# Optimization experiments

Hardware: AMD Instinct MI355X
Metric: run time of the kernel (lower is better)

Reference implementation:

```python
import jax, jax.numpy as jnp
import numpy as np

B, IN, OUT = 8192, 1024, 1024


def setup_inputs() -> dict:
    key = jax.random.key(0)
    k1, k2 = jax.random.split(key)
    x = jax.random.normal(k1, (B, IN), dtype=jnp.float32)
    W_seed = jax.random.normal(k2, (IN, OUT), dtype=jnp.float32) / np.sqrt(IN).astype(np.float32)
    b_seed = jnp.zeros((OUT,), dtype=jnp.float32)
    W_sig = jnp.zeros((2,), dtype=jnp.float32)  # mixture logits over ['dense','Toeplitz']
    b_sig = jnp.zeros((2,), dtype=jnp.float32)  # mixture logits over ['dense','None']
    A_sig = jnp.zeros((2,), dtype=jnp.float32)  # mixture logits over ['linear','relu']
    return {"x": x, "W_seed": W_seed, "b_seed": b_seed,
            "W_sig": W_sig, "b_sig": b_sig, "A_sig": A_sig}


def _toeplitz_from_seed(W_seed):
    # seed_vec = [W_seed[0, out-1], ..., W_seed[0, 1], W_seed[0,0], ..., W_seed[in-1,0]]
    in_sz, out_sz = W_seed.shape
    seed_vec = jnp.concatenate([W_seed[0, -1:0:-1], W_seed[:, 0]])  # [out-1 + in]
    # W_toep[i, j] = seed_vec[i - j + out - 1]
    idx = jnp.arange(in_sz)[:, None] - jnp.arange(out_sz)[None, :] + (out_sz - 1)
    return seed_vec[idx]  # [in, out]


def reference(x, W_seed, b_seed, W_sig, b_sig, A_sig):
    W_toep = _toeplitz_from_seed(W_seed)
    w_s = jax.nn.softmax(W_sig)
    W_core = w_s[0] * W_seed + w_s[1] * W_toep          # softmax-weighted weight mixture
    b_s = jax.nn.softmax(b_sig)
    b_core = b_s[0] * b_seed                             # 'None' branch contributes zeros
    out = x @ W_core + b_core                            # [B, out]
    a_s = jax.nn.softmax(A_sig)
    return a_s[0] * out + a_s[1] * jax.nn.relu(out)      # activation mixture
```

## Files before the change

### kernel.cpp

```cpp
#include <hip/hip_runtime.h>

typedef unsigned short ushort_t;
typedef __bf16 bf16x8 __attribute__((ext_vector_type(8)));
typedef float f32x4 __attribute__((ext_vector_type(4)));

#define AS1 __attribute__((address_space(1)))
#define AS3 __attribute__((address_space(3)))

__device__ __forceinline__ ushort_t f2bf(float f) {
    unsigned u = __builtin_bit_cast(unsigned, f);
    u = (u + 0x7fffu + ((u >> 16) & 1u)) >> 16;
    return (ushort_t)u;
}

__device__ __forceinline__ void async16(void* lds, const void* g) {
    __builtin_amdgcn_global_load_lds((const AS1 unsigned int*)g,
                                     (AS3 unsigned int*)lds, 16, 0, 0);
}

__device__ __forceinline__ void softmax2(const float* __restrict__ sig, float& s0, float& s1) {
    float a = sig[0], b = sig[1];
    float m = fmaxf(a, b);
    float e0 = __expf(a - m), e1 = __expf(b - m);
    float inv = 1.0f / (e0 + e1);
    s0 = e0 * inv; s1 = e1 * inv;
}

__device__ __forceinline__ float toep_val(const float* __restrict__ Wseed, int k, int o) {
    return (k >= o) ? Wseed[(size_t)(k - o) << 10] : Wseed[o - k];
}

__global__ __launch_bounds__(256) void prep_kernel(const float* __restrict__ x,
                                                   const float* __restrict__ Wseed,
                                                   const float* __restrict__ Wsig,
                                                   ushort_t* __restrict__ xb,
                                                   ushort_t* __restrict__ Wt) {
    int b = blockIdx.x;
    if (b < 4096) {
        int i = b * 256 + threadIdx.x;
        const float4* xp = (const float4*)x + (size_t)i * 2;
        float4 a = xp[0], c = xp[1];
        uint4 r;
        r.x = (unsigned)f2bf(a.x) | ((unsigned)f2bf(a.y) << 16);
        r.y = (unsigned)f2bf(a.z) | ((unsigned)f2bf(a.w) << 16);
        r.z = (unsigned)f2bf(c.x) | ((unsigned)f2bf(c.y) << 16);
        r.w = (unsigned)f2bf(c.z) | ((unsigned)f2bf(c.w) << 16);
        ((uint4*)xb)[i] = r;
        return;
    }
    __shared__ float T[64][65];
    int bb = b - 4096;
    int k0 = (bb >> 4) * 64;
    int o0 = (bb & 15) * 64;
    int t = threadIdx.x;
    #pragma unroll
    for (int i = 0; i < 4; ++i) {
        int lin = t + i * 256;
        int kr = lin >> 4;
        int c4 = lin & 15;
        float4 v = *(const float4*)&Wseed[(size_t)(k0 + kr) * 1024 + o0 + c4 * 4];
        T[kr][c4 * 4 + 0] = v.x;
        T[kr][c4 * 4 + 1] = v.y;
        T[kr][c4 * 4 + 2] = v.z;
        T[kr][c4 * 4 + 3] = v.w;
    }
    __syncthreads();
    float s0, s1; softmax2(Wsig, s0, s1);
    #pragma unroll
    for (int i = 0; i < 2; ++i) {
        int lin = t + i * 256;
        int oo = lin >> 3;
        int kq = (lin & 7) * 8;
        unsigned r[4];
        #pragma unroll
        for (int q = 0; q < 4; ++q) {
            float v0 = s0 * T[kq + 2 * q + 0][oo] + s1 * toep_val(Wseed, k0 + kq + 2 * q + 0, o0 + oo);
            float v1 = s0 * T[kq + 2 * q + 1][oo] + s1 * toep_val(Wseed, k0 + kq + 2 * q + 1, o0 + oo);
            r[q] = (unsigned)f2bf(v0) | ((unsigned)f2bf(v1) << 16);
        }
        *(uint4*)&Wt[(size_t)(o0 + oo) * 1024 + k0 + kq] = make_uint4(r[0], r[1], r[2], r[3]);
    }
}

#define NKT 16

__global__ __launch_bounds__(512, 2) void gemm_kernel(const ushort_t* __restrict__ Xb,
                                                      const ushort_t* __restrict__ Wt,
                                                      const float* __restrict__ bseed,
                                                      const float* __restrict__ bsig,
                                                      const float* __restrict__ asig,
                                                      float* __restrict__ out) {
    __shared__ ushort_t lds[73728];
    ushort_t* p0 = lds;
    ushort_t* p1 = lds + 24576;
    ushort_t* p2 = lds + 49152;

    const int t = threadIdx.x;
    const int wv = t >> 6;
    const int lane = t & 63;

    const int orig = blockIdx.x;
    const int g = orig & 7;
    const int within = orig >> 3;
    const int rb = g * 4 + (within >> 3);
    const int cb = within & 7;
    const int brow = rb * 256;
    const int bcol = cb * 128;

    const int r0 = t >> 3;
    const int kcs = 8 * ((t & 7) ^ (r0 & 7));
    const ushort_t* gA = Xb + (size_t)(brow + r0) * 1024 + kcs;
    const ushort_t* gB = Wt + (size_t)(bcol + r0) * 1024 + kcs;

    const int wr = (wv >> 1) * 64;
    const int wcn = (wv & 1) * 64;
    const int fr = lane & 15;
    const int kg = (lane >> 4) * 8;
    const int frx = (fr & 7) << 3;

    f32x4 acc[4][4];
    #pragma unroll
    for (int i = 0; i < 4; ++i)
        #pragma unroll
        for (int j = 0; j < 4; ++j) acc[i][j] = (f32x4){0.f, 0.f, 0.f, 0.f};
    bf16x8 bfr[4][2];

    float bs0, bs1, as0, as1;
    softmax2(bsig, bs0, bs1);
    softmax2(asig, as0, as1);
    float bias[4];
    #pragma unroll
    for (int ni = 0; ni < 4; ++ni)
        bias[ni] = bs0 * bseed[bcol + wcn + ni * 16 + fr];
    asm volatile("" :: "v"(bias[0]), "v"(bias[1]), "v"(bias[2]), "v"(bias[3]),
                       "v"(as0), "v"(as1));
    asm volatile("" ::: "memory");

#define PH(p, STAGEBLK)                                                            \
    do {                                                                           \
        const int arow_ = wr + (p) * 16 + fr;                                      \
        bf16x8 a0 = *(const bf16x8*)&p0[arow_ * 64 + ((0 + kg) ^ frx)];            \
        bf16x8 a1 = *(const bf16x8*)&p0[arow_ * 64 + ((32 + kg) ^ frx)];           \
        if ((p) == 0) {                                                            \
            _Pragma("unroll")                                                      \
            for (int ni = 0; ni < 4; ++ni) {                                       \
                int br_ = wcn + ni * 16 + fr;                                      \
                bfr[ni][0] = *(const bf16x8*)&p0[16384 + br_ * 64 + ((0 + kg) ^ frx)];  \
                bfr[ni][1] = *(const bf16x8*)&p0[16384 + br_ * 64 + ((32 + kg) ^ frx)]; \
            }                                                                      \
        }                                                                          \
        STAGEBLK                                                                   \
        asm volatile("" ::: "memory");                                             \
        __builtin_amdgcn_s_barrier();                                              \
        __builtin_amdgcn_s_setprio(1);                                             \
        _Pragma("unroll")                                                          \
        for (int ni = 0; ni < 4; ++ni) {                                           \
            acc[p][ni] = __builtin_amdgcn_mfma_f32_16x16x32_bf16(a0, bfr[ni][0],   \
                                                                 acc[p][ni], 0, 0, 0); \
            acc[p][ni] = __builtin_amdgcn_mfma_f32_16x16x32_bf16(a1, bfr[ni][1],   \
                                                                 acc[p][ni], 0, 0, 0); \
        }                                                                          \
        __builtin_amdgcn_s_setprio(0);                                             \
    } while (0)

    async16(p0 + wv * 512,          gA);
    async16(p0 + 4096 + wv * 512,   gA + 65536);
    async16(p0 + 8192 + wv * 512,   gA + 131072);
    async16(p0 + 12288 + wv * 512,  gA + 196608);
    async16(p0 + 16384 + wv * 512,  gB);
    async16(p0 + 20480 + wv * 512,  gB + 65536);
    async16(p1 + wv * 512,          gA + 64);
    async16(p1 + 4096 + wv * 512,   gA + 65536 + 64);
    async16(p1 + 8192 + wv * 512,   gA + 131072 + 64);
    async16(p1 + 12288 + wv * 512,  gA + 196608 + 64);
    async16(p1 + 16384 + wv * 512,  gB + 64);
    async16(p1 + 20480 + wv * 512,  gB + 65536 + 64);
    asm volatile("s_waitcnt vmcnt(6)" ::: "memory");
    __builtin_amdgcn_s_barrier();

    for (int T = 0; T < NKT; ++T) {
        const size_t t2 = (size_t)(T + 2) * 64;
        const bool dost = (T < NKT - 2);
        PH(0, { if (dost) { async16(p2 + wv * 512,          gA + t2);
                            async16(p2 + 4096 + wv * 512,   gA + 65536 + t2); } });
        __builtin_amdgcn_s_barrier();
        PH(1, { if (dost) { async16(p2 + 8192 + wv * 512,   gA + 131072 + t2);
                            async16(p2 + 12288 + wv * 512,  gA + 196608 + t2); } });
        __builtin_amdgcn_s_barrier();
        PH(2, { if (dost) { async16(p2 + 16384 + wv * 512,  gB + t2);
                            async16(p2 + 20480 + wv * 512,  gB + 65536 + t2); } });
        __builtin_amdgcn_s_barrier();
        PH(3, {});
        if (T < NKT - 2)        { asm volatile("s_waitcnt vmcnt(6)" ::: "memory"); }
        else if (T == NKT - 2)  { asm volatile("s_waitcnt vmcnt(0)" ::: "memory"); }
        __builtin_amdgcn_s_barrier();
        ushort_t* tmp_ = p0; p0 = p1; p1 = p2; p2 = tmp_;
    }

    #pragma unroll
    for (int ni = 0; ni < 4; ++ni) {
        int col = bcol + wcn + ni * 16 + fr;
        #pragma unroll
        for (int mi = 0; mi < 4; ++mi) {
            int row = brow + wr + mi * 16 + (lane >> 4) * 4;
            #pragma unroll
            for (int r = 0; r < 4; ++r) {
                float v = acc[mi][ni][r] + bias[ni];
                out[(size_t)(row + r) * 1024 + col] = as0 * v + as1 * fmaxf(v, 0.f);
            }
        }
    }
#undef PH
}

__global__ __launch_bounds__(256) void naive_kernel(const float* __restrict__ x,
                                                    const float* __restrict__ Wseed,
                                                    const float* __restrict__ bseed,
                                                    const float* __restrict__ Wsig,
                                                    const float* __restrict__ bsig,
                                                    const float* __restrict__ asig,
                                                    float* __restrict__ out) {
    int idx = blockIdx.x * 256 + threadIdx.x;
    int b = idx >> 10, o = idx & 1023;
    float ws0, ws1, bs0, bs1, as0, as1;
    softmax2(Wsig, ws0, ws1);
    softmax2(bsig, bs0, bs1);
    softmax2(asig, as0, as1);
    float s = 0.f;
    const float* xr = x + (size_t)b * 1024;
    for (int k = 0; k < 1024; ++k) {
        float wc = ws0 * Wseed[((size_t)k << 10) + o] + ws1 * toep_val(Wseed, k, o);
        s += xr[k] * wc;
    }
    float v = s + bs0 * bseed[o];
    out[idx] = as0 * v + as1 * fmaxf(v, 0.f);
}

extern "C" void kernel_launch(void* const* d_in, const int* in_sizes, int n_in,
                              void* d_out, int out_size, void* d_ws, size_t ws_size,
                              hipStream_t stream) {
    const float* x     = (const float*)d_in[0];
    const float* Wseed = (const float*)d_in[1];
    const float* bseed = (const float*)d_in[2];
    const float* Wsig  = (const float*)d_in[3];
    const float* bsig  = (const float*)d_in[4];
    const float* Asig  = (const float*)d_in[5];
    float* out = (float*)d_out;

    const size_t need = (2u << 20) + (16u << 20) + 1024;
    if (ws_size < need) {
        naive_kernel<<<dim3(8192 * 1024 / 256), dim3(256), 0, stream>>>(
            x, Wseed, bseed, Wsig, bsig, Asig, out);
        return;
    }

    ushort_t* Wt = (ushort_t*)d_ws;
    ushort_t* Xb = (ushort_t*)((char*)d_ws + (2u << 20));

    prep_kernel<<<dim3(4096 + 256), dim3(256), 0, stream>>>(x, Wseed, Wsig, Xb, Wt);
    gemm_kernel<<<dim3(256), dim3(512), 0, stream>>>(Xb, Wt, bseed, bsig, Asig, out);
}
```

Before: 44.38 us.

## Fuse fp32-to-bf16 conversion of X into GEMM A-tile loading

Removes the separate pass that converted x to bf16 in a workspace. The GEMM now loads fp32 x tiles into registers one K-step ahead, converts them in-kernel and writes bf16 into LDS, while B still streams asynchronously via global_load_lds. This saves a 32MB read plus 16MB write-and-reread of the bf16 copy. In exchange it adds register pressure (launch bounds relaxed to one block per SM) and synchronous LDS writes in the main loop.

Result: faster. 40.08 us (-9.7%).

```diff
diff --git a/kernel.cpp b/kernel.cpp
--- a/kernel.cpp
+++ b/kernel.cpp
@@ -30,26 +30,11 @@
     return (k >= o) ? Wseed[(size_t)(k - o) << 10] : Wseed[o - k];
 }
 
-__global__ __launch_bounds__(256) void prep_kernel(const float* __restrict__ x,
-                                                   const float* __restrict__ Wseed,
-                                                   const float* __restrict__ Wsig,
-                                                   ushort_t* __restrict__ xb,
-                                                   ushort_t* __restrict__ Wt) {
-    int b = blockIdx.x;
-    if (b < 4096) {
-        int i = b * 256 + threadIdx.x;
-        const float4* xp = (const float4*)x + (size_t)i * 2;
-        float4 a = xp[0], c = xp[1];
-        uint4 r;
-        r.x = (unsigned)f2bf(a.x) | ((unsigned)f2bf(a.y) << 16);
-        r.y = (unsigned)f2bf(a.z) | ((unsigned)f2bf(a.w) << 16);
-        r.z = (unsigned)f2bf(c.x) | ((unsigned)f2bf(c.y) << 16);
-        r.w = (unsigned)f2bf(c.z) | ((unsigned)f2bf(c.w) << 16);
-        ((uint4*)xb)[i] = r;
-        return;
-    }
+__global__ __launch_bounds__(256) void prep_w_kernel(const float* __restrict__ Wseed,
+                                                     const float* __restrict__ Wsig,
+                                                     ushort_t* __restrict__ Wt) {
     __shared__ float T[64][65];
-    int bb = b - 4096;
+    int bb = blockIdx.x;
     int k0 = (bb >> 4) * 64;
     int o0 = (bb & 15) * 64;
     int t = threadIdx.x;
@@ -84,7 +69,7 @@
 
 #define NKT 16
 
-__global__ __launch_bounds__(512, 2) void gemm_kernel(const ushort_t* __restrict__ Xb,
+__global__ __launch_bounds__(512, 1) void gemm_kernel(const float* __restrict__ Xf,
                                                       const ushort_t* __restrict__ Wt,
                                                       const float* __restrict__ bseed,
                                                       const float* __restrict__ bsig,
@@ -109,8 +94,8 @@
 
     const int r0 = t >> 3;
     const int kcs = 8 * ((t & 7) ^ (r0 & 7));
-    const ushort_t* gA = Xb + (size_t)(brow + r0) * 1024 + kcs;
-    const ushort_t* gB = Wt + (size_t)(bcol + r0) * 1024 + kcs;
+    const float*    gXf = Xf + (size_t)(brow + r0) * 1024 + kcs;
+    const ushort_t* gB  = Wt + (size_t)(bcol + r0) * 1024 + kcs;
 
     const int wr = (wv >> 1) * 64;
     const int wcn = (wv & 1) * 64;
@@ -124,6 +109,7 @@
         #pragma unroll
         for (int j = 0; j < 4; ++j) acc[i][j] = (f32x4){0.f, 0.f, 0.f, 0.f};
     bf16x8 bfr[4][2];
+    f32x4 ar[8];
 
     float bs0, bs1, as0, as1;
     softmax2(bsig, bs0, bs1);
@@ -135,6 +121,26 @@
     asm volatile("" :: "v"(bias[0]), "v"(bias[1]), "v"(bias[2]), "v"(bias[3]),
                        "v"(as0), "v"(as1));
     asm volatile("" ::: "memory");
+
+#define LOADA2(g0, koff)                                                           \
+    do {                                                                           \
+        ar[2*(g0)]   = *(const f32x4*)(gXf + (g0) * 65536 + (koff));               \
+        ar[2*(g0)+1] = *(const f32x4*)(gXf + (g0) * 65536 + (koff) + 4);           \
+    } while (0)
+
+#define WRITEA(dstA)                                                               \
+    do {                                                                           \
+        _Pragma("unroll")                                                          \
+        for (int g_ = 0; g_ < 4; ++g_) {                                           \
+            bf16x8 v_;                                                             \
+            _Pragma("unroll")                                                      \
+            for (int j_ = 0; j_ < 4; ++j_) {                                       \
+                v_[j_]     = (__bf16)ar[2 * g_][j_];                               \
+                v_[4 + j_] = (__bf16)ar[2 * g_ + 1][j_];                           \
+            }                                                                      \
+            *(bf16x8*)&(dstA)[g_ * 4096 + t * 8] = v_;                             \
+        }                                                                          \
+    } while (0)
 
 #define PH(p, STAGEBLK)                                                            \
     do {                                                                           \
@@ -163,36 +169,34 @@
         __builtin_amdgcn_s_setprio(0);                                             \
     } while (0)
 
-    async16(p0 + wv * 512,          gA);
-    async16(p0 + 4096 + wv * 512,   gA + 65536);
-    async16(p0 + 8192 + wv * 512,   gA + 131072);
-    async16(p0 + 12288 + wv * 512,  gA + 196608);
-    async16(p0 + 16384 + wv * 512,  gB);
-    async16(p0 + 20480 + wv * 512,  gB + 65536);
-    async16(p1 + wv * 512,          gA + 64);
-    async16(p1 + 4096 + wv * 512,   gA + 65536 + 64);
-    async16(p1 + 8192 + wv * 512,   gA + 131072 + 64);
-    async16(p1 + 12288 + wv * 512,  gA + 196608 + 64);
-    async16(p1 + 16384 + wv * 512,  gB + 64);
-    async16(p1 + 20480 + wv * 512,  gB + 65536 + 64);
-    asm volatile("s_waitcnt vmcnt(6)" ::: "memory");
+    LOADA2(0, 0); LOADA2(1, 0); LOADA2(2, 0); LOADA2(3, 0);
+    async16(p0 + 16384 + wv * 512, gB);
+    async16(p0 + 20480 + wv * 512, gB + 65536);
+    async16(p1 + 16384 + wv * 512, gB + 64);
+    async16(p1 + 20480 + wv * 512, gB + 65536 + 64);
+    asm volatile("s_waitcnt vmcnt(4)" ::: "memory");
+    __builtin_amdgcn_sched_barrier(0);
+    WRITEA(p0);
+    asm volatile("s_waitcnt vmcnt(2)" ::: "memory");
+    asm volatile("s_waitcnt lgkmcnt(0)" ::: "memory");
     __builtin_amdgcn_s_barrier();
 
     for (int T = 0; T < NKT; ++T) {
-        const size_t t2 = (size_t)(T + 2) * 64;
-        const bool dost = (T < NKT - 2);
-        PH(0, { if (dost) { async16(p2 + wv * 512,          gA + t2);
-                            async16(p2 + 4096 + wv * 512,   gA + 65536 + t2); } });
-        __builtin_amdgcn_s_barrier();
-        PH(1, { if (dost) { async16(p2 + 8192 + wv * 512,   gA + 131072 + t2);
-                            async16(p2 + 12288 + wv * 512,  gA + 196608 + t2); } });
-        __builtin_amdgcn_s_barrier();
-        PH(2, { if (dost) { async16(p2 + 16384 + wv * 512,  gB + t2);
-                            async16(p2 + 20480 + wv * 512,  gB + 65536 + t2); } });
+        const size_t ka = (size_t)(T + 1) * 64;
+        const size_t kb = (size_t)(T + 2) * 64;
+        PH(0, { if (T < NKT - 1) { LOADA2(0, ka); LOADA2(1, ka); } });
+        __builtin_amdgcn_s_barrier();
+        PH(1, { if (T < NKT - 1) { LOADA2(2, ka); LOADA2(3, ka); } });
+        __builtin_amdgcn_s_barrier();
+        PH(2, { if (T < NKT - 2) { async16(p2 + 16384 + wv * 512, gB + kb);
+                                   async16(p2 + 20480 + wv * 512, gB + 65536 + kb); } });
         __builtin_amdgcn_s_barrier();
         PH(3, {});
-        if (T < NKT - 2)        { asm volatile("s_waitcnt vmcnt(6)" ::: "memory"); }
-        else if (T == NKT - 2)  { asm volatile("s_waitcnt vmcnt(0)" ::: "memory"); }
+        if (T < NKT - 2)       { asm volatile("s_waitcnt vmcnt(2)" ::: "memory"); }
+        else if (T == NKT - 2) { asm volatile("s_waitcnt vmcnt(0)" ::: "memory"); }
+        __builtin_amdgcn_sched_barrier(0);
+        if (T < NKT - 1) WRITEA(p1);
+        asm volatile("s_waitcnt lgkmcnt(0)" ::: "memory");
         __builtin_amdgcn_s_barrier();
         ushort_t* tmp_ = p0; p0 = p1; p1 = p2; p2 = tmp_;
     }
@@ -211,6 +215,8 @@
         }
     }
 #undef PH
+#undef LOADA2
+#undef WRITEA
 }
 
 __global__ __launch_bounds__(256) void naive_kernel(const float* __restrict__ x,
@@ -247,7 +253,7 @@
     const float* Asig  = (const float*)d_in[5];
     float* out = (float*)d_out;
 
-    const size_t need = (2u << 20) + (16u << 20) + 1024;
+    const size_t need = (2u << 20) + 1024;
     if (ws_size < need) {
         naive_kernel<<<dim3(8192 * 1024 / 256), dim3(256), 0, stream>>>(
             x, Wseed, bseed, Wsig, bsig, Asig, out);
@@ -255,8 +261,7 @@
     }
 
     ushort_t* Wt = (ushort_t*)d_ws;
-    ushort_t* Xb = (ushort_t*)((char*)d_ws + (2u << 20));
-
-    prep_kernel<<<dim3(4096 + 256), dim3(256), 0, stream>>>(x, Wseed, Wsig, Xb, Wt);
-    gemm_kernel<<<dim3(256), dim3(512), 0, stream>>>(Xb, Wt, bseed, bsig, Asig, out);
-}
+
+    prep_w_kernel<<<dim3(256), dim3(256), 0, stream>>>(Wseed, Wsig, Wt);
+    gemm_kernel<<<dim3(256), dim3(512), 0, stream>>>(x, Wt, bseed, bsig, Asig, out);
+}
```
